# Kernel tuning notes

Measured on AMD Instinct MI355X. Metric: run time of the kernel, lower is better.

## Reference

```python
import jax, jax.numpy as jnp
import numpy as np

N_NODES = 50000
N_EDGES = 1600000
F_IN = 384
NR_SIGMOID = 1  # hidden_sizes[-1]


def setup_inputs() -> dict:
    key = jax.random.key(0)
    ks = jax.random.split(key, 8)
    x = jax.random.normal(ks[0], (N_NODES, F_IN), jnp.float32)
    edge_index = jax.random.randint(ks[1], (2, N_EDGES), 0, N_NODES, jnp.int32)
    def lin(k, fin, fout):
        return jax.random.normal(k, (fin, fout), jnp.float32) / np.sqrt(fin).astype(np.float32)
    W1 = lin(ks[2], F_IN, 64)
    W2 = lin(ks[3], 64, 32)
    W3 = lin(ks[4], 32, 1 + F_IN)  # reconstruction=True: last width = 1 + input_size
    return {
        "x": x, "edge_index": edge_index,
        "W1": W1, "b1": jnp.zeros((64,), jnp.float32),
        "W2": W2, "b2": jnp.zeros((32,), jnp.float32),
        "W3": W3, "b3": jnp.zeros((1 + F_IN,), jnp.float32),
    }


def reference(x, edge_index, W1, b1, W2, b2, W3, b3):
    N = x.shape[0]
    self_loop = jnp.arange(N, dtype=edge_index.dtype)
    src = jnp.concatenate([edge_index[0], self_loop])  # [E+N]
    dst = jnp.concatenate([edge_index[1], self_loop])
    # symmetric GCN normalization (with self-loops), as in PyG GCNConv
    deg = jax.ops.segment_sum(jnp.ones(dst.shape[0], x.dtype), dst, num_segments=N)
    dinv = jnp.where(deg > 0, jax.lax.rsqrt(deg), 0.0)
    norm = (dinv[src] * dinv[dst])[:, None]  # [E+N, 1]

    def gcn_conv(h, W, b):
        m = h @ W                         # transform first (fewer message bytes)
        agg = jax.ops.segment_sum(m[src] * norm, dst, num_segments=N)
        return agg + b

    h = jax.nn.relu(gcn_conv(x, W1, b1))
    h = jax.nn.relu(gcn_conv(h, W2, b2))
    h = gcn_conv(h, W3, b3)
    # sigmoid on the first nr_sigmoid_layers columns only
    return jnp.concatenate([jax.nn.sigmoid(h[:, :NR_SIGMOID]), h[:, NR_SIGMOID:]], axis=1)
```

## Files before the change

kernel.cpp:

```cpp
#include <hip/hip_runtime.h>

#define F_IN  384
#define EPB   4096
#define NBINS 256
#define BCAP  10240
#define SDS   208

typedef __attribute__((ext_vector_type(8))) short short8v;
typedef __attribute__((ext_vector_type(4))) float f32x4;

__device__ __forceinline__ unsigned short f2bf(float f) {
    unsigned u = __float_as_uint(f);
    return (unsigned short)((u + 0x7FFFu + ((u >> 16) & 1u)) >> 16);
}
__device__ __forceinline__ float bflo(unsigned u) { return __uint_as_float(u << 16); }
__device__ __forceinline__ float bfhi(unsigned u) { return __uint_as_float(u & 0xFFFF0000u); }


__launch_bounds__(256)
__global__ void k_p1(const int* __restrict__ ei, int E, int NBK,
                     unsigned* __restrict__ packed, unsigned short* __restrict__ segdesc) {
    __shared__ unsigned sin[EPB];
    __shared__ unsigned sout[EPB];
    __shared__ int hist[257], cur[256], excl[257];
    const int t = threadIdx.x;
    const int e0 = blockIdx.x * EPB;
    const int cnt = min(EPB, E - e0);

    if (t < 256) { hist[t] = 0; cur[t] = 0; }
    if (t == 0) hist[256] = 0;
    __syncthreads();

    for (int i = t; i < cnt; i += 256) {
        int s = ei[e0 + i];
        int d = ei[E + e0 + i];
        sin[i] = ((unsigned)d << 16) | (unsigned)s;
        atomicAdd(&hist[d >> 8], 1);
    }
    __syncthreads();

    if (t < 64) {
        int carry = 0;
        for (int c = 0; c * 64 < NBK; ++c) {
            int idx = c * 64 + t;
            int v = (idx < NBK) ? hist[idx] : 0;
            int x = v;
#pragma unroll
            for (int d = 1; d < 64; d <<= 1) { int y = __shfl_up(x, d, 64); if (t >= d) x += y; }
            if (idx < NBK) excl[idx] = carry + x - v;
            carry += __shfl(x, 63, 64);
        }
        if (t == 0) excl[NBK] = carry;
    }
    __syncthreads();

    for (int i = t; i < cnt; i += 256) {
        unsigned v = sin[i];
        int b = v >> 24;
        int pos = excl[b] + atomicAdd(&cur[b], 1);
        sout[pos] = v;
    }
    __syncthreads();

    for (int i = t; i < cnt; i += 256) packed[(size_t)e0 + i] = sout[i];
    for (int i = t; i <= NBK; i += 256) segdesc[(size_t)blockIdx.x * SDS + i] = (unsigned short)excl[i];
}


__launch_bounds__(256)
__global__ void k_p2(const unsigned* __restrict__ packed, const unsigned short* __restrict__ segdesc,
                     int NB1, unsigned short* __restrict__ eidx,
                     int* __restrict__ rpB, int* __restrict__ rpE,
                     float* __restrict__ dinv, int N) {
    __shared__ unsigned ev[BCAP];
    __shared__ unsigned short se[BCAP];
    __shared__ int lenS[512], offS[513], srcS[512];
    __shared__ int hist[NBINS], cur[NBINS], excl[NBINS + 1];
    const int t = threadIdx.x;
    const int b = blockIdx.x;

    if (t < NBINS) { hist[t] = 0; cur[t] = 0; }
    for (int blk = t; blk < NB1; blk += 256) {
        int s0 = segdesc[(size_t)blk * SDS + b];
        int s1 = segdesc[(size_t)blk * SDS + b + 1];
        lenS[blk] = s1 - s0;
        srcS[blk] = s0;
    }
    __syncthreads();

    if (t < 64) {
        int carry = 0;
        for (int c = 0; c * 64 < NB1; ++c) {
            int idx = c * 64 + t;
            int v = (idx < NB1) ? lenS[idx] : 0;
            int x = v;
#pragma unroll
            for (int d = 1; d < 64; d <<= 1) { int y = __shfl_up(x, d, 64); if (t >= d) x += y; }
            if (idx < NB1) offS[idx] = carry + x - v;
            carry += __shfl(x, 63, 64);
        }
        if (t == 0) offS[NB1 < 512 ? NB1 : 512] = carry;
    }
    __syncthreads();
    const int total = min(offS[NB1 < 512 ? NB1 : 512], BCAP);

    for (int blk = t; blk < NB1; blk += 256) {
        int l = lenS[blk], o = offS[blk];
        if (o + l > BCAP) l = max(0, BCAP - o);
        const unsigned* sp = packed + (size_t)blk * EPB + srcS[blk];
        for (int j = 0; j < l; ++j) ev[o + j] = sp[j];
    }
    __syncthreads();

    for (int i = t; i < total; i += 256) atomicAdd(&hist[(ev[i] >> 16) & 0xFF], 1);
    __syncthreads();

    if (t < 64) {
        int carry = 0;
#pragma unroll
        for (int c = 0; c < 4; ++c) {
            int idx = c * 64 + t;
            int v = hist[idx];
            int x = v;
#pragma unroll
            for (int d = 1; d < 64; d <<= 1) { int y = __shfl_up(x, d, 64); if (t >= d) x += y; }
            excl[idx] = carry + x - v;
            carry += __shfl(x, 63, 64);
        }
        if (t == 0) excl[NBINS] = carry;
    }
    __syncthreads();

    if (t < NBINS) {
        int d = b * NBINS + t;
        if (d < N) {
            int c = hist[t];
            int base = b * BCAP + excl[t];
            rpB[d] = base;
            rpE[d] = base + c;
            dinv[d] = rsqrtf((float)(c + 1));
        }
    }
    for (int i = t; i < total; i += 256) {
        unsigned v = ev[i];
        int l = (v >> 16) & 0xFF;
        int p = excl[l] + atomicAdd(&cur[l], 1);
        se[p] = (unsigned short)(v & 0xFFFF);
    }
    __syncthreads();
    for (int i = t; i < total; i += 256) eidx[(size_t)b * BCAP + i] = se[i];
}


__global__ void k_wt(const float* __restrict__ W1, const float* __restrict__ W3,
                     unsigned short* __restrict__ w1t, unsigned short* __restrict__ w3t) {
    int idx = blockIdx.x * 256 + threadIdx.x;
    if (idx < 384 * 64) {
        int k = idx >> 6, col = idx & 63;
        w1t[(size_t)col * 384 + k] = f2bf(W1[idx]);
    }
    int j = idx - 384 * 64;
    if (j >= 0 && j < 384 * 32) {
        int col = j >> 5, k = j & 31;
        w3t[(size_t)col * 32 + k] = f2bf(W3[(size_t)k * 385 + col]);
    }
}


__launch_bounds__(256)
__global__ void k_gemm1(const float* __restrict__ x, const unsigned short* __restrict__ w1t,
                        const float* __restrict__ dinv,
                        unsigned short* __restrict__ m1p, int N) {
    __shared__ __align__(16) unsigned short xb[32][136];
    const int t    = threadIdx.x;
    const int lane = t & 63;
    const int wv   = t >> 6;
    const int lr   = lane & 15;
    const int kg   = lane >> 4;
    const int row0 = blockIdx.x * 32;
    const int col  = (wv << 4) + lr;

    short8v bf[12];
    const unsigned short* wcol = w1t + (size_t)col * 384 + (kg << 3);
#pragma unroll
    for (int c = 0; c < 12; c++)
        bf[c] = *reinterpret_cast<const short8v*>(&wcol[c * 32]);

    int sr[2], sk[2];
    const float* sp[2];
    bool sv[2];
#pragma unroll
    for (int i = 0; i < 2; i++) {
        int g = t + i * 256;
        sr[i] = g >> 4;
        sk[i] = (g & 15) << 3;
        int row = row0 + sr[i];
        sv[i] = (row < N);
        sp[i] = x + (size_t)row * F_IN + sk[i];
    }

    float4 preA0, preA1, preB0, preB1;
    preA0 = sv[0] ? *reinterpret_cast<const float4*>(sp[0])     : make_float4(0, 0, 0, 0);
    preA1 = sv[0] ? *reinterpret_cast<const float4*>(sp[0] + 4) : make_float4(0, 0, 0, 0);
    preB0 = sv[1] ? *reinterpret_cast<const float4*>(sp[1])     : make_float4(0, 0, 0, 0);
    preB1 = sv[1] ? *reinterpret_cast<const float4*>(sp[1] + 4) : make_float4(0, 0, 0, 0);

    f32x4 acc0 = (f32x4){0.f, 0.f, 0.f, 0.f};
    f32x4 acc1 = (f32x4){0.f, 0.f, 0.f, 0.f};

    for (int k0 = 0; k0 < F_IN; k0 += 128) {
        __syncthreads();
        {
            short8v p;
            p[0] = (short)f2bf(preA0.x); p[1] = (short)f2bf(preA0.y);
            p[2] = (short)f2bf(preA0.z); p[3] = (short)f2bf(preA0.w);
            p[4] = (short)f2bf(preA1.x); p[5] = (short)f2bf(preA1.y);
            p[6] = (short)f2bf(preA1.z); p[7] = (short)f2bf(preA1.w);
            *reinterpret_cast<short8v*>(&xb[sr[0]][sk[0]]) = p;
            p[0] = (short)f2bf(preB0.x); p[1] = (short)f2bf(preB0.y);
            p[2] = (short)f2bf(preB0.z); p[3] = (short)f2bf(preB0.w);
            p[4] = (short)f2bf(preB1.x); p[5] = (short)f2bf(preB1.y);
            p[6] = (short)f2bf(preB1.z); p[7] = (short)f2bf(preB1.w);
            *reinterpret_cast<short8v*>(&xb[sr[1]][sk[1]]) = p;
        }
        if (k0 + 128 < F_IN) {
            const float* q0 = sp[0] + k0 + 128;
            const float* q1 = sp[1] + k0 + 128;
            preA0 = sv[0] ? *reinterpret_cast<const float4*>(q0)     : make_float4(0, 0, 0, 0);
            preA1 = sv[0] ? *reinterpret_cast<const float4*>(q0 + 4) : make_float4(0, 0, 0, 0);
            preB0 = sv[1] ? *reinterpret_cast<const float4*>(q1)     : make_float4(0, 0, 0, 0);
            preB1 = sv[1] ? *reinterpret_cast<const float4*>(q1 + 4) : make_float4(0, 0, 0, 0);
        }
        __syncthreads();

#pragma unroll
        for (int kk = 0; kk < 4; kk++) {
            const int c = (k0 >> 5) + kk;
            short8v a0 = *reinterpret_cast<const short8v*>(&xb[lr][(kk << 5) + (kg << 3)]);
            short8v a1 = *reinterpret_cast<const short8v*>(&xb[16 + lr][(kk << 5) + (kg << 3)]);
            acc0 = __builtin_amdgcn_mfma_f32_16x16x32_bf16(a0, bf[c], acc0, 0, 0, 0);
            acc1 = __builtin_amdgcn_mfma_f32_16x16x32_bf16(a1, bf[c], acc1, 0, 0, 0);
        }
    }

    const size_t hbase = (size_t)(col >> 5) * ((size_t)N * 32) + (col & 31);
#pragma unroll
    for (int i = 0; i < 4; i++) {
        int rowA = row0 + (kg << 2) + i;
        if (rowA < N) m1p[hbase + (size_t)rowA * 32] = f2bf(acc0[i] * dinv[rowA]);
        int rowB = row0 + 16 + (kg << 2) + i;
        if (rowB < N) m1p[hbase + (size_t)rowB * 32] = f2bf(acc1[i] * dinv[rowB]);
    }
}


__launch_bounds__(256)
__global__ void k_g64half(const int* __restrict__ rpB, const int* __restrict__ rpE,
                          const unsigned short* __restrict__ eidx,
                          const unsigned* __restrict__ msg,
                          const float* __restrict__ b1h,
                          const float* __restrict__ dinv,
                          unsigned* __restrict__ m1h,
                          int houtoff, int N) {
    int w = blockIdx.x * 16 + (threadIdx.x >> 4);
    if (w >= N) return;
    int f = threadIdx.x & 15;
    int i = rpB[w], e = rpE[w];
    unsigned u = msg[(size_t)w * 16 + f];
    float l0 = bflo(u), h0 = bfhi(u);
    float l1 = 0.f, h1 = 0.f, l2 = 0.f, h2 = 0.f, l3 = 0.f, h3 = 0.f;
    float l4 = 0.f, h4 = 0.f, l5 = 0.f, h5 = 0.f, l6 = 0.f, h6 = 0.f, l7 = 0.f, h7 = 0.f;
    for (; i + 8 <= e; i += 8) {
        unsigned u0 = msg[(size_t)eidx[i]     * 16 + f];
        unsigned u1 = msg[(size_t)eidx[i + 1] * 16 + f];
        unsigned u2 = msg[(size_t)eidx[i + 2] * 16 + f];
        unsigned u3 = msg[(size_t)eidx[i + 3] * 16 + f];
        unsigned u4 = msg[(size_t)eidx[i + 4] * 16 + f];
        unsigned u5 = msg[(size_t)eidx[i + 5] * 16 + f];
        unsigned u6 = msg[(size_t)eidx[i + 6] * 16 + f];
        unsigned u7 = msg[(size_t)eidx[i + 7] * 16 + f];
        l0 += bflo(u0); h0 += bfhi(u0);  l1 += bflo(u1); h1 += bfhi(u1);
        l2 += bflo(u2); h2 += bfhi(u2);  l3 += bflo(u3); h3 += bfhi(u3);
        l4 += bflo(u4); h4 += bfhi(u4);  l5 += bflo(u5); h5 += bfhi(u5);
        l6 += bflo(u6); h6 += bfhi(u6);  l7 += bflo(u7); h7 += bfhi(u7);
    }
    for (; i + 4 <= e; i += 4) {
        unsigned u0 = msg[(size_t)eidx[i]     * 16 + f];
        unsigned u1 = msg[(size_t)eidx[i + 1] * 16 + f];
        unsigned u2 = msg[(size_t)eidx[i + 2] * 16 + f];
        unsigned u3 = msg[(size_t)eidx[i + 3] * 16 + f];
        l0 += bflo(u0); h0 += bfhi(u0);  l1 += bflo(u1); h1 += bfhi(u1);
        l2 += bflo(u2); h2 += bfhi(u2);  l3 += bflo(u3); h3 += bfhi(u3);
    }
    for (; i < e; i++) {
        unsigned u0 = msg[(size_t)eidx[i] * 16 + f];
        l0 += bflo(u0); h0 += bfhi(u0);
    }
    float suml = ((l0 + l1) + (l2 + l3)) + ((l4 + l5) + (l6 + l7));
    float sumh = ((h0 + h1) + (h2 + h3)) + ((h4 + h5) + (h6 + h7));
    float s = dinv[w];
    float hl = fmaxf(suml * s + b1h[(f << 1)], 0.f);
    float hh = fmaxf(sumh * s + b1h[(f << 1) + 1], 0.f);
    m1h[(size_t)w * 32 + houtoff + f] = (unsigned)f2bf(hl) | ((unsigned)f2bf(hh) << 16);
}


__launch_bounds__(256)
__global__ void k_gather32h(const int* __restrict__ rpB, const int* __restrict__ rpE,
                            const unsigned short* __restrict__ eidx,
                            const unsigned* __restrict__ msg,
                            void* __restrict__ outp, int N,
                            const float* __restrict__ bias, const float* __restrict__ dinv,
                            const float* __restrict__ W3, const float* __restrict__ b3,
                            float* __restrict__ out) {
    int w = blockIdx.x * 16 + (threadIdx.x >> 4);
    if (w >= N) return;
    int f = threadIdx.x & 15;
    int i = rpB[w], e = rpE[w];
    unsigned u = msg[(size_t)w * 16 + f];
    float l0 = bflo(u), h0 = bfhi(u);
    float l1 = 0.f, h1 = 0.f, l2 = 0.f, h2 = 0.f, l3 = 0.f, h3 = 0.f;
    float l4 = 0.f, h4 = 0.f, l5 = 0.f, h5 = 0.f, l6 = 0.f, h6 = 0.f, l7 = 0.f, h7 = 0.f;
    for (; i + 8 <= e; i += 8) {
        unsigned u0 = msg[(size_t)eidx[i]     * 16 + f];
        unsigned u1 = msg[(size_t)eidx[i + 1] * 16 + f];
        unsigned u2 = msg[(size_t)eidx[i + 2] * 16 + f];
        unsigned u3 = msg[(size_t)eidx[i + 3] * 16 + f];
        unsigned u4 = msg[(size_t)eidx[i + 4] * 16 + f];
        unsigned u5 = msg[(size_t)eidx[i + 5] * 16 + f];
        unsigned u6 = msg[(size_t)eidx[i + 6] * 16 + f];
        unsigned u7 = msg[(size_t)eidx[i + 7] * 16 + f];
        l0 += bflo(u0); h0 += bfhi(u0);  l1 += bflo(u1); h1 += bfhi(u1);
        l2 += bflo(u2); h2 += bfhi(u2);  l3 += bflo(u3); h3 += bfhi(u3);
        l4 += bflo(u4); h4 += bfhi(u4);  l5 += bflo(u5); h5 += bfhi(u5);
        l6 += bflo(u6); h6 += bfhi(u6);  l7 += bflo(u7); h7 += bfhi(u7);
    }
    for (; i + 4 <= e; i += 4) {
        unsigned u0 = msg[(size_t)eidx[i]     * 16 + f];
        unsigned u1 = msg[(size_t)eidx[i + 1] * 16 + f];
        unsigned u2 = msg[(size_t)eidx[i + 2] * 16 + f];
        unsigned u3 = msg[(size_t)eidx[i + 3] * 16 + f];
        l0 += bflo(u0); h0 += bfhi(u0);  l1 += bflo(u1); h1 += bfhi(u1);
        l2 += bflo(u2); h2 += bfhi(u2);  l3 += bflo(u3); h3 += bfhi(u3);
    }
    for (; i < e; i++) {
        unsigned u0 = msg[(size_t)eidx[i] * 16 + f];
        l0 += bflo(u0); h0 += bfhi(u0);
    }
    float rl = ((l0 + l1) + (l2 + l3)) + ((l4 + l5) + (l6 + l7));
    float rh = ((h0 + h1) + (h2 + h3)) + ((h4 + h5) + (h6 + h7));
    float s = dinv[w];
    if (bias) {
        rl = fmaxf(rl * s + bias[(f << 1)], 0.f) * s;
        rh = fmaxf(rh * s + bias[(f << 1) + 1], 0.f) * s;
        ((unsigned*)outp)[(size_t)w * 16 + f] = (unsigned)f2bf(rl) | ((unsigned)f2bf(rh) << 16);
    } else {
        float gl = rl * s, gh = rh * s;
        ((unsigned*)outp)[(size_t)w * 16 + f] = (unsigned)f2bf(gl) | ((unsigned)f2bf(gh) << 16);
        float p = gl * W3[(size_t)(2 * f) * 385 + 384] + gh * W3[(size_t)(2 * f + 1) * 385 + 384];
#pragma unroll
        for (int m = 8; m >= 1; m >>= 1) p += __shfl_xor(p, m, 64);
        if (f == 0) out[(size_t)w * 385 + 384] = p + b3[384];
    }
}


__launch_bounds__(256)
__global__ void k_layer2(const unsigned* __restrict__ m1h, const float* __restrict__ W2,
                         const float* __restrict__ dinv,
                         unsigned short* __restrict__ m2p, int N) {
    const int t    = threadIdx.x;
    const int lane = t & 63;
    const int wv   = t >> 6;
    const int lr   = lane & 15;
    const int kg   = lane >> 4;
    const int row0 = blockIdx.x * 64 + (wv << 4);

    short8v b00, b01, b10, b11;
#pragma unroll
    for (int j = 0; j < 8; j++) {
        int k = (kg << 3) + j;
        b00[j] = (short)f2bf(W2[(size_t)k * 32 + lr]);
        b01[j] = (short)f2bf(W2[(size_t)k * 32 + 16 + lr]);
        b10[j] = (short)f2bf(W2[(size_t)(32 + k) * 32 + lr]);
        b11[j] = (short)f2bf(W2[(size_t)(32 + k) * 32 + 16 + lr]);
    }

    int arow = row0 + lr;
    short8v a0 = (short8v){0, 0, 0, 0, 0, 0, 0, 0};
    short8v a1 = (short8v){0, 0, 0, 0, 0, 0, 0, 0};
    if (arow < N) {
        a0 = *reinterpret_cast<const short8v*>(&m1h[(size_t)arow * 32 + (kg << 2)]);
        a1 = *reinterpret_cast<const short8v*>(&m1h[(size_t)arow * 32 + 16 + (kg << 2)]);
    }

    f32x4 accA = (f32x4){0.f, 0.f, 0.f, 0.f};
    f32x4 accB = (f32x4){0.f, 0.f, 0.f, 0.f};
    accA = __builtin_amdgcn_mfma_f32_16x16x32_bf16(a0, b00, accA, 0, 0, 0);
    accA = __builtin_amdgcn_mfma_f32_16x16x32_bf16(a1, b10, accA, 0, 0, 0);
    accB = __builtin_amdgcn_mfma_f32_16x16x32_bf16(a0, b01, accB, 0, 0, 0);
    accB = __builtin_amdgcn_mfma_f32_16x16x32_bf16(a1, b11, accB, 0, 0, 0);

#pragma unroll
    for (int i = 0; i < 4; i++) {
        int row = row0 + (kg << 2) + i;
        if (row < N) {
            float s = dinv[row];
            m2p[(size_t)row * 32 + lr]      = f2bf(accA[i] * s);
            m2p[(size_t)row * 32 + 16 + lr] = f2bf(accB[i] * s);
        }
    }
}


__launch_bounds__(256)
__global__ void k_out(const unsigned* __restrict__ gbf, const unsigned short* __restrict__ w3t,
                      const float* __restrict__ b3, float* __restrict__ out, int N) {
    const int t    = threadIdx.x;
    const int lane = t & 63;
    const int wv   = t >> 6;
    const int lr   = lane & 15;
    const int kg   = lane >> 4;
    const int row0 = blockIdx.x * 64;
    const int col  = blockIdx.y * 64 + (wv << 4) + lr;

    short8v bfrag = *reinterpret_cast<const short8v*>(&w3t[(size_t)col * 32 + (kg << 3)]);
    const float bias = b3[col];

#pragma unroll
    for (int rb = 0; rb < 4; rb++) {
        int arow = row0 + (rb << 4) + lr;
        short8v afrag = (short8v){0, 0, 0, 0, 0, 0, 0, 0};
        if (arow < N)
            afrag = *reinterpret_cast<const short8v*>(&gbf[(size_t)arow * 16 + (kg << 2)]);
        f32x4 acc = (f32x4){0.f, 0.f, 0.f, 0.f};
        acc = __builtin_amdgcn_mfma_f32_16x16x32_bf16(afrag, bfrag, acc, 0, 0, 0);
#pragma unroll
        for (int i = 0; i < 4; i++) {
            int row = row0 + (rb << 4) + (kg << 2) + i;
            if (row < N) {
                float v = acc[i] + bias;
                if (col == 0) v = 1.0f / (1.0f + expf(-v));
                out[(size_t)row * 385 + col] = v;
            }
        }
    }
}

extern "C" void kernel_launch(void* const* d_in, const int* in_sizes, int n_in,
                              void* d_out, int out_size, void* d_ws, size_t ws_size,
                              hipStream_t stream) {
    const float* x  = (const float*)d_in[0];
    const int*   ei = (const int*)d_in[1];
    const float* W1 = (const float*)d_in[2];
    const float* b1 = (const float*)d_in[3];
    const float* W2 = (const float*)d_in[4];
    const float* b2 = (const float*)d_in[5];
    const float* W3 = (const float*)d_in[6];
    const float* b3 = (const float*)d_in[7];
    float* out = (float*)d_out;

    const int N = in_sizes[0] / F_IN;
    const int E = in_sizes[1] / 2;
    const int NB1 = (E + EPB - 1) / EPB;
    const int NBK = (N + NBINS - 1) / NBINS;

    float* ws   = (float*)d_ws;
    float* dinv = ws;
    float* bufA = ws + N;
    float* bufB = bufA + (size_t)64 * N;
    int*   rpB  = (int*)(bufB + (size_t)64 * N);
    int*   rpE  = rpB + N;
    unsigned short* eidx    = (unsigned short*)(rpE + N);
    unsigned short* segdesc = eidx + (size_t)NBK * BCAP;
    unsigned short* w1t     = segdesc + (size_t)NB1 * SDS;
    unsigned short* w3t     = w1t + (size_t)64 * 384;

    unsigned* packed = (unsigned*)bufA;
    unsigned short* m1p = (unsigned short*)bufA;
    unsigned* m1h = (unsigned*)bufB;
    unsigned short* m2p = (unsigned short*)bufA;
    unsigned short* h2p = (unsigned short*)bufB;
    unsigned* gbf = (unsigned*)(bufA + (size_t)32 * N);

    k_p1<<<NB1, 256, 0, stream>>>(ei, E, NBK, packed, segdesc);
    k_p2<<<NBK, 256, 0, stream>>>(packed, segdesc, NB1, eidx, rpB, rpE, dinv, N);
    k_wt<<<(384 * 64 + 384 * 32 + 255) / 256, 256, 0, stream>>>(W1, W3, w1t, w3t);

    k_gemm1  <<<(N + 31) / 32, 256, 0, stream>>>(x, w1t, dinv, m1p, N);
    k_g64half<<<(N + 15) / 16, 256, 0, stream>>>(rpB, rpE, eidx,
                                                 (const unsigned*)m1p,                       b1,      dinv, m1h,  0, N);
    k_g64half<<<(N + 15) / 16, 256, 0, stream>>>(rpB, rpE, eidx,
                                                 (const unsigned*)(m1p + (size_t)N * 32),    b1 + 32, dinv, m1h, 16, N);

    k_layer2  <<<(N + 63) / 64, 256, 0, stream>>>(m1h, W2, dinv, m2p, N);
    k_gather32h<<<(N + 15) / 16, 256, 0, stream>>>(rpB, rpE, eidx, (const unsigned*)m2p,
                                                   (void*)h2p, N, b2, dinv, nullptr, nullptr, nullptr);

    k_gather32h<<<(N + 15) / 16, 256, 0, stream>>>(rpB, rpE, eidx, (const unsigned*)h2p,
                                                   (void*)gbf, N, nullptr, dinv, W3, b3, out);

    dim3 gout((N + 63) / 64, 6);
    k_out<<<gout, 256, 0, stream>>>(gbf, w3t, b3, out, N);
}
```

Measured before the change: 151.0 us.

## Fuse final gather with output GEMM and merge weight transpose into partition kernel

The last aggregation of layer 3 and the 32x385 output projection now run in one kernel. Each block gathers 64 nodes with 4 threads per node doing 16-byte loads, stages the bf16 rows in shared memory, then runs the MFMA for all six column tiles. The separate weight-transpose kernel is folded into extra blocks of the edge-partition kernel. This removes two launches and the global round trip of the intermediate buffer, but the gather now uses only 4 threads per node with fewer accumulators, which may lower memory-level parallelism.

```diff
diff --git a/kernel.cpp b/kernel.cpp
--- a/kernel.cpp
+++ b/kernel.cpp
@@ -5,6 +5,7 @@
 #define NBINS 256
 #define BCAP  10240
 #define SDS   208
+#define WTBLK 144
 
 typedef __attribute__((ext_vector_type(8))) short short8v;
 typedef __attribute__((ext_vector_type(4))) float f32x4;
@@ -18,12 +19,30 @@
 
 
 __launch_bounds__(256)
-__global__ void k_p1(const int* __restrict__ ei, int E, int NBK,
-                     unsigned* __restrict__ packed, unsigned short* __restrict__ segdesc) {
+__global__ void k_p1(const int* __restrict__ ei, int E, int NBK, int NB1,
+                     unsigned* __restrict__ packed, unsigned short* __restrict__ segdesc,
+                     const float* __restrict__ W1, const float* __restrict__ W3,
+                     unsigned short* __restrict__ w1t, unsigned short* __restrict__ w3t) {
     __shared__ unsigned sin[EPB];
     __shared__ unsigned sout[EPB];
     __shared__ int hist[257], cur[256], excl[257];
     const int t = threadIdx.x;
+
+    if (blockIdx.x >= NB1) {
+        int idx = (blockIdx.x - NB1) * 256 + t;
+        if (idx < 384 * 64) {
+            int k = idx >> 6, col = idx & 63;
+            w1t[(size_t)col * 384 + k] = f2bf(W1[idx]);
+        } else {
+            int j = idx - 384 * 64;
+            if (j < 384 * 32) {
+                int col = j >> 5, k = j & 31;
+                w3t[(size_t)col * 32 + k] = f2bf(W3[(size_t)k * 385 + col]);
+            }
+        }
+        return;
+    }
+
     const int e0 = blockIdx.x * EPB;
     const int cnt = min(EPB, E - e0);
 
@@ -149,21 +168,6 @@
     }
     __syncthreads();
     for (int i = t; i < total; i += 256) eidx[(size_t)b * BCAP + i] = se[i];
-}
-
-
-__global__ void k_wt(const float* __restrict__ W1, const float* __restrict__ W3,
-                     unsigned short* __restrict__ w1t, unsigned short* __restrict__ w3t) {
-    int idx = blockIdx.x * 256 + threadIdx.x;
-    if (idx < 384 * 64) {
-        int k = idx >> 6, col = idx & 63;
-        w1t[(size_t)col * 384 + k] = f2bf(W1[idx]);
-    }
-    int j = idx - 384 * 64;
-    if (j >= 0 && j < 384 * 32) {
-        int col = j >> 5, k = j & 31;
-        w3t[(size_t)col * 32 + k] = f2bf(W3[(size_t)k * 385 + col]);
-    }
 }
 
 
@@ -309,10 +313,8 @@
 __global__ void k_gather32h(const int* __restrict__ rpB, const int* __restrict__ rpE,
                             const unsigned short* __restrict__ eidx,
                             const unsigned* __restrict__ msg,
-                            void* __restrict__ outp, int N,
-                            const float* __restrict__ bias, const float* __restrict__ dinv,
-                            const float* __restrict__ W3, const float* __restrict__ b3,
-                            float* __restrict__ out) {
+                            unsigned* __restrict__ outp, int N,
+                            const float* __restrict__ bias, const float* __restrict__ dinv) {
     int w = blockIdx.x * 16 + (threadIdx.x >> 4);
     if (w >= N) return;
     int f = threadIdx.x & 15;
@@ -350,18 +352,9 @@
     float rl = ((l0 + l1) + (l2 + l3)) + ((l4 + l5) + (l6 + l7));
     float rh = ((h0 + h1) + (h2 + h3)) + ((h4 + h5) + (h6 + h7));
     float s = dinv[w];
-    if (bias) {
-        rl = fmaxf(rl * s + bias[(f << 1)], 0.f) * s;
-        rh = fmaxf(rh * s + bias[(f << 1) + 1], 0.f) * s;
-        ((unsigned*)outp)[(size_t)w * 16 + f] = (unsigned)f2bf(rl) | ((unsigned)f2bf(rh) << 16);
-    } else {
-        float gl = rl * s, gh = rh * s;
-        ((unsigned*)outp)[(size_t)w * 16 + f] = (unsigned)f2bf(gl) | ((unsigned)f2bf(gh) << 16);
-        float p = gl * W3[(size_t)(2 * f) * 385 + 384] + gh * W3[(size_t)(2 * f + 1) * 385 + 384];
-#pragma unroll
-        for (int m = 8; m >= 1; m >>= 1) p += __shfl_xor(p, m, 64);
-        if (f == 0) out[(size_t)w * 385 + 384] = p + b3[384];
-    }
+    rl = fmaxf(rl * s + bias[(f << 1)], 0.f) * s;
+    rh = fmaxf(rh * s + bias[(f << 1) + 1], 0.f) * s;
+    outp[(size_t)w * 16 + f] = (unsigned)f2bf(rl) | ((unsigned)f2bf(rh) << 16);
 }
 
 
@@ -414,34 +407,86 @@
 
 
 __launch_bounds__(256)
-__global__ void k_out(const unsigned* __restrict__ gbf, const unsigned short* __restrict__ w3t,
-                      const float* __restrict__ b3, float* __restrict__ out, int N) {
+__global__ void k_g32out(const int* __restrict__ rpB, const int* __restrict__ rpE,
+                         const unsigned short* __restrict__ eidx,
+                         const uint4* __restrict__ msg,
+                         const float* __restrict__ dinv,
+                         const unsigned short* __restrict__ w3t,
+                         const float* __restrict__ W3, const float* __restrict__ b3,
+                         float* __restrict__ out, int N) {
+    __shared__ unsigned g[64][16];
     const int t    = threadIdx.x;
+    const int row0 = blockIdx.x * 64;
+    const int wn   = t >> 2;
+    const int q    = t & 3;
+    const int w    = row0 + wn;
+
+    if (w < N) {
+        int i = rpB[w], e = rpE[w];
+        uint4 u = msg[(size_t)w * 4 + q];
+        float a0 = bflo(u.x), a1 = bfhi(u.x), a2 = bflo(u.y), a3 = bfhi(u.y);
+        float a4 = bflo(u.z), a5 = bfhi(u.z), a6 = bflo(u.w), a7 = bfhi(u.w);
+        float c0 = 0.f, c1 = 0.f, c2 = 0.f, c3 = 0.f, c4 = 0.f, c5 = 0.f, c6 = 0.f, c7 = 0.f;
+        for (; i + 4 <= e; i += 4) {
+            uint4 v0 = msg[(size_t)eidx[i]     * 4 + q];
+            uint4 v1 = msg[(size_t)eidx[i + 1] * 4 + q];
+            uint4 v2 = msg[(size_t)eidx[i + 2] * 4 + q];
+            uint4 v3 = msg[(size_t)eidx[i + 3] * 4 + q];
+            a0 += bflo(v0.x); a1 += bfhi(v0.x); a2 += bflo(v0.y); a3 += bfhi(v0.y);
+            a4 += bflo(v0.z); a5 += bfhi(v0.z); a6 += bflo(v0.w); a7 += bfhi(v0.w);
+            c0 += bflo(v1.x); c1 += bfhi(v1.x); c2 += bflo(v1.y); c3 += bfhi(v1.y);
+            c4 += bflo(v1.z); c5 += bfhi(v1.z); c6 += bflo(v1.w); c7 += bfhi(v1.w);
+            a0 += bflo(v2.x); a1 += bfhi(v2.x); a2 += bflo(v2.y); a3 += bfhi(v2.y);
+            a4 += bflo(v2.z); a5 += bfhi(v2.z); a6 += bflo(v2.w); a7 += bfhi(v2.w);
+            c0 += bflo(v3.x); c1 += bfhi(v3.x); c2 += bflo(v3.y); c3 += bfhi(v3.y);
+            c4 += bflo(v3.z); c5 += bfhi(v3.z); c6 += bflo(v3.w); c7 += bfhi(v3.w);
+        }
+        for (; i < e; i++) {
+            uint4 v0 = msg[(size_t)eidx[i] * 4 + q];
+            a0 += bflo(v0.x); a1 += bfhi(v0.x); a2 += bflo(v0.y); a3 += bfhi(v0.y);
+            a4 += bflo(v0.z); a5 += bfhi(v0.z); a6 += bflo(v0.w); a7 += bfhi(v0.w);
+        }
+        float s = dinv[w];
+        float g0 = (a0 + c0) * s, g1 = (a1 + c1) * s, g2 = (a2 + c2) * s, g3 = (a3 + c3) * s;
+        float g4 = (a4 + c4) * s, g5 = (a5 + c5) * s, g6 = (a6 + c6) * s, g7 = (a7 + c7) * s;
+        g[wn][q * 4 + 0] = (unsigned)f2bf(g0) | ((unsigned)f2bf(g1) << 16);
+        g[wn][q * 4 + 1] = (unsigned)f2bf(g2) | ((unsigned)f2bf(g3) << 16);
+        g[wn][q * 4 + 2] = (unsigned)f2bf(g4) | ((unsigned)f2bf(g5) << 16);
+        g[wn][q * 4 + 3] = (unsigned)f2bf(g6) | ((unsigned)f2bf(g7) << 16);
+        const float* wc = W3 + (size_t)(8 * q) * 385 + 384;
+        float p = g0 * wc[0] + g1 * wc[385] + g2 * wc[2 * 385] + g3 * wc[3 * 385]
+                + g4 * wc[4 * 385] + g5 * wc[5 * 385] + g6 * wc[6 * 385] + g7 * wc[7 * 385];
+        p += __shfl_xor(p, 1, 64);
+        p += __shfl_xor(p, 2, 64);
+        if (q == 0) out[(size_t)w * 385 + 384] = p + b3[384];
+    } else {
+        g[wn][q * 4 + 0] = 0; g[wn][q * 4 + 1] = 0;
+        g[wn][q * 4 + 2] = 0; g[wn][q * 4 + 3] = 0;
+    }
+    __syncthreads();
+
     const int lane = t & 63;
     const int wv   = t >> 6;
     const int lr   = lane & 15;
     const int kg   = lane >> 4;
-    const int row0 = blockIdx.x * 64;
-    const int col  = blockIdx.y * 64 + (wv << 4) + lr;
-
-    short8v bfrag = *reinterpret_cast<const short8v*>(&w3t[(size_t)col * 32 + (kg << 3)]);
-    const float bias = b3[col];
-
-#pragma unroll
-    for (int rb = 0; rb < 4; rb++) {
-        int arow = row0 + (rb << 4) + lr;
-        short8v afrag = (short8v){0, 0, 0, 0, 0, 0, 0, 0};
-        if (arow < N)
-            afrag = *reinterpret_cast<const short8v*>(&gbf[(size_t)arow * 16 + (kg << 2)]);
-        f32x4 acc = (f32x4){0.f, 0.f, 0.f, 0.f};
-        acc = __builtin_amdgcn_mfma_f32_16x16x32_bf16(afrag, bfrag, acc, 0, 0, 0);
-#pragma unroll
-        for (int i = 0; i < 4; i++) {
-            int row = row0 + (rb << 4) + (kg << 2) + i;
-            if (row < N) {
-                float v = acc[i] + bias;
-                if (col == 0) v = 1.0f / (1.0f + expf(-v));
-                out[(size_t)row * 385 + col] = v;
+#pragma unroll
+    for (int y = 0; y < 6; y++) {
+        int col = y * 64 + (wv << 4) + lr;
+        short8v bfrag = *reinterpret_cast<const short8v*>(&w3t[(size_t)col * 32 + (kg << 3)]);
+        float bias = b3[col];
+#pragma unroll
+        for (int rb = 0; rb < 4; rb++) {
+            short8v afrag = *reinterpret_cast<const short8v*>(&g[(rb << 4) + lr][kg << 2]);
+            f32x4 acc = (f32x4){0.f, 0.f, 0.f, 0.f};
+            acc = __builtin_amdgcn_mfma_f32_16x16x32_bf16(afrag, bfrag, acc, 0, 0, 0);
+#pragma unroll
+            for (int i = 0; i < 4; i++) {
+                int row = row0 + (rb << 4) + (kg << 2) + i;
+                if (row < N) {
+                    float v = acc[i] + bias;
+                    if (col == 0) v = 1.0f / (1.0f + expf(-v));
+                    out[(size_t)row * 385 + col] = v;
+                }
             }
         }
     }
@@ -481,25 +526,20 @@
     unsigned* m1h = (unsigned*)bufB;
     unsigned short* m2p = (unsigned short*)bufA;
     unsigned short* h2p = (unsigned short*)bufB;
-    unsigned* gbf = (unsigned*)(bufA + (size_t)32 * N);
-
-    k_p1<<<NB1, 256, 0, stream>>>(ei, E, NBK, packed, segdesc);
+
+    k_p1<<<NB1 + WTBLK, 256, 0, stream>>>(ei, E, NBK, NB1, packed, segdesc, W1, W3, w1t, w3t);
     k_p2<<<NBK, 256, 0, stream>>>(packed, segdesc, NB1, eidx, rpB, rpE, dinv, N);
-    k_wt<<<(384 * 64 + 384 * 32 + 255) / 256, 256, 0, stream>>>(W1, W3, w1t, w3t);
 
     k_gemm1  <<<(N + 31) / 32, 256, 0, stream>>>(x, w1t, dinv, m1p, N);
     k_g64half<<<(N + 15) / 16, 256, 0, stream>>>(rpB, rpE, eidx,
-                                                 (const unsigned*)m1p,                       b1,      dinv, m1h,  0, N);
+                                                 (const unsigned*)m1p,                    b1,      dinv, m1h,  0, N);
     k_g64half<<<(N + 15) / 16, 256, 0, stream>>>(rpB, rpE, eidx,
-                                                 (const unsigned*)(m1p + (size_t)N * 32),    b1 + 32, dinv, m1h, 16, N);
+                                                 (const unsigned*)(m1p + (size_t)N * 32), b1 + 32, dinv, m1h, 16, N);
 
     k_layer2  <<<(N + 63) / 64, 256, 0, stream>>>(m1h, W2, dinv, m2p, N);
     k_gather32h<<<(N + 15) / 16, 256, 0, stream>>>(rpB, rpE, eidx, (const unsigned*)m2p,
-                                                   (void*)h2p, N, b2, dinv, nullptr, nullptr, nullptr);
-
-    k_gather32h<<<(N + 15) / 16, 256, 0, stream>>>(rpB, rpE, eidx, (const unsigned*)h2p,
-                                                   (void*)gbf, N, nullptr, dinv, W3, b3, out);
-
-    dim3 gout((N + 63) / 64, 6);
-    k_out<<<gout, 256, 0, stream>>>(gbf, w3t, b3, out, N);
-}
+                                                   (unsigned*)h2p, N, b2, dinv);
+
+    k_g32out<<<(N + 63) / 64, 256, 0, stream>>>(rpB, rpE, eidx, (const uint4*)h2p, dinv,
+                                                w3t, W3, b3, out, N);
+}
```

After: 145.1 us, median of 2. -3.9%, faster.
